# Performance work log

Measured on AMD Instinct MI355X. Metric: run time of the kernel, lower is better.

## Reference

```python
import jax, jax.numpy as jnp
import numpy as np

D_MODEL = 1024
NUM_HEADS = 16
D_K = D_MODEL // NUM_HEADS
LOCAL_WINDOW = 256
SCALE = 1.0 / np.float32(np.sqrt(D_K))
NEG = -1e9


def setup_inputs() -> dict:
    key = jax.random.key(0)
    ks = jax.random.split(key, 11)
    B, S, D = 2, 2048, D_MODEL
    s = 1.0 / np.float32(np.sqrt(D))
    return {
        "query": jax.random.normal(ks[0], (B, S, D), jnp.float32),
        "key": jax.random.normal(ks[1], (B, S, D), jnp.float32),
        "value": jax.random.normal(ks[2], (B, S, D), jnp.float32),
        "Wq": jax.random.normal(ks[3], (D, D), jnp.float32) * s,
        "bq": jnp.zeros((D,), jnp.float32),
        "Wk": jax.random.normal(ks[4], (D, D), jnp.float32) * s,
        "bk": jnp.zeros((D,), jnp.float32),
        "Wv": jax.random.normal(ks[5], (D, D), jnp.float32) * s,
        "bv": jnp.zeros((D,), jnp.float32),
        "Wo": jax.random.normal(ks[6], (D, D), jnp.float32) * s,
        "bo": jnp.zeros((D,), jnp.float32),
    }


def _band_mask(S):
    # torch loop: allowed cols j with max(0, i - w//2) <= j < min(S, i + w//2)
    i = jnp.arange(S)
    diff = i[None, :] - i[:, None]  # j - i
    half = LOCAL_WINDOW // 2
    return (diff >= -half) & (diff < half)  # [S, S] bool


def reference(query, key, value, Wq, bq, Wk, bk, Wv, bv, Wo, bo):
    B, S, D = query.shape
    H, dk = NUM_HEADS, D_K

    def proj(x, W, b):
        # nn.Linear: x @ W.T + b ; then split heads -> [B, H, S, dk]
        return (x @ W.T + b).reshape(B, S, H, dk).transpose(0, 2, 1, 3)

    Q = proj(query, Wq, bq)
    K = proj(key, Wk, bk)
    V = proj(value, Wv, bv)

    scores = jnp.einsum("bhqd,bhkd->bhqk", Q, K) * SCALE  # [B,H,S,S]
    band = _band_mask(S)
    scores = jnp.where(band[None, None, :, :], scores, NEG)
    attn = jax.nn.softmax(scores, axis=-1)
    out = jnp.einsum("bhqk,bhkd->bhqd", attn, V)  # [B,H,S,dk]
    out = out.transpose(0, 2, 1, 3).reshape(B, S, D)
    return out @ Wo.T + bo
```

## Files before the change

kernel.cpp:

```cpp
#include <hip/hip_runtime.h>
#include <stdint.h>

#define S_LEN 2048
#define NB 2
#define NH 16
#define DK 64
#define DM 1024
#define QK_SCALE 0.125f
#define NEG_BIG -1e30f

typedef __attribute__((ext_vector_type(8))) short bf16x8;
typedef __attribute__((ext_vector_type(4))) float f32x4;

static __device__ __forceinline__ f32x4 mfma16(bf16x8 a, bf16x8 b, f32x4 c) {
    return __builtin_amdgcn_mfma_f32_16x16x32_bf16(a, b, c, 0, 0, 0);
}

static __device__ __forceinline__ void gload_lds16(const void* g, void* l) {
    __builtin_amdgcn_global_load_lds((const __attribute__((address_space(1))) void*)g,
                                     (__attribute__((address_space(3))) void*)l,
                                     16, 0, 0);
}

static __device__ __forceinline__ unsigned short f2bf(float x) {
    unsigned int u = __float_as_uint(x);
    u += 0x7fffu + ((u >> 16) & 1u);
    return (unsigned short)(u >> 16);
}

struct CvtArgs {
    const float* src[7];
    unsigned short* dst[7];
    int n8[7];
};

__global__ __launch_bounds__(256) void cvt_f32_bf16(CvtArgs a) {
    const int t = blockIdx.y;
    const float* __restrict__ src = a.src[t];
    unsigned short* __restrict__ dst = a.dst[t];
    const int n8 = a.n8[t];
    const int stride = gridDim.x * blockDim.x;
    for (int i = blockIdx.x * blockDim.x + threadIdx.x; i < n8; i += stride) {
        float4 v0 = ((const float4*)src)[(size_t)i * 2];
        float4 v1 = ((const float4*)src)[(size_t)i * 2 + 1];
        union { bf16x8 v; unsigned short h[8]; } u;
        u.h[0] = f2bf(v0.x); u.h[1] = f2bf(v0.y); u.h[2] = f2bf(v0.z); u.h[3] = f2bf(v0.w);
        u.h[4] = f2bf(v1.x); u.h[5] = f2bf(v1.y); u.h[6] = f2bf(v1.z); u.h[7] = f2bf(v1.w);
        ((bf16x8*)dst)[i] = u.v;
    }
}

static __device__ __forceinline__ void gemm_core_128(
    const unsigned short* __restrict__ A,
    const unsigned short* __restrict__ W,
    unsigned short* sA, unsigned short* sB,
    int K, int m0, int n0, f32x4 acc[4][4])
{
    const int tid = threadIdx.x;
    const int wid = tid >> 6, lane = tid & 63;
    const int wr = wid >> 1, wc = wid & 1;
    const int fr = lane & 15, fg = lane >> 4;
    const int ldr = lane >> 3;
    const int ldc = ((lane & 7) ^ (lane >> 3)) * 8;

    const unsigned short* pA = A + (size_t)(m0 + ldr) * K + ldc;
    const unsigned short* pW = W + (size_t)(n0 + ldr) * K + ldc;

    const int cka0 = ((0 + fg) ^ (fr & 7)) * 8;
    const int cka1 = ((4 + fg) ^ (fr & 7)) * 8;

    for (int k0 = 0; k0 < K; k0 += 64) {
        __syncthreads();
        #pragma unroll
        for (int it = 0; it < 4; ++it) {
            const int rb = wid * 32 + it * 8;
            gload_lds16(pA + (size_t)(rb)*K + k0, sA + rb * 64);
            gload_lds16(pW + (size_t)(rb)*K + k0, sB + rb * 64);
        }
        __syncthreads();
        #pragma unroll
        for (int kf = 0; kf < 2; ++kf) {
            const int cka = kf ? cka1 : cka0;
            bf16x8 af[4], bfr[4];
            #pragma unroll
            for (int mf = 0; mf < 4; ++mf)
                af[mf] = *(const bf16x8*)(sA + (wr * 64 + mf * 16 + fr) * 64 + cka);
            #pragma unroll
            for (int nf = 0; nf < 4; ++nf)
                bfr[nf] = *(const bf16x8*)(sB + (wc * 64 + nf * 16 + fr) * 64 + cka);
            #pragma unroll
            for (int mf = 0; mf < 4; ++mf)
                #pragma unroll
                for (int nf = 0; nf < 4; ++nf)
                    acc[mf][nf] = mfma16(af[mf], bfr[nf], acc[mf][nf]);
        }
    }
}

__global__ __launch_bounds__(256, 3) void gemm_qkv(
    const unsigned short* __restrict__ Xq, const unsigned short* __restrict__ Xk,
    const unsigned short* __restrict__ Xv,
    const unsigned short* __restrict__ Wq, const unsigned short* __restrict__ Wk,
    const unsigned short* __restrict__ Wv,
    const float* __restrict__ bq, const float* __restrict__ bk, const float* __restrict__ bv,
    unsigned short* __restrict__ Qo, unsigned short* __restrict__ Ko,
    unsigned short* __restrict__ Vt)
{
    __shared__ unsigned short sA[128 * 64];
    __shared__ unsigned short sB[128 * 64];
    const int z = blockIdx.z;
    const unsigned short* A = (z == 0) ? Xq : ((z == 1) ? Xk : Xv);
    const unsigned short* W = (z == 0) ? Wq : ((z == 1) ? Wk : Wv);
    const float* bias = (z == 0) ? bq : ((z == 1) ? bk : bv);
    const int m0 = blockIdx.y * 128, n0 = blockIdx.x * 128;

    f32x4 acc[4][4] = {};
    gemm_core_128(A, W, sA, sB, DM, m0, n0, acc);

    const int tid = threadIdx.x, wid = tid >> 6, lane = tid & 63;
    const int wr = wid >> 1, wc = wid & 1, fr = lane & 15, fg = lane >> 4;
    unsigned short* Oh = (z == 0) ? Qo : Ko;
    #pragma unroll
    for (int nf = 0; nf < 4; ++nf) {
        const int col = n0 + wc * 64 + nf * 16 + fr;
        const float bb = bias[col];
        const int h = col >> 6, dd = col & (DK - 1);
        #pragma unroll
        for (int mf = 0; mf < 4; ++mf) {
            #pragma unroll
            for (int r = 0; r < 4; ++r) {
                const int row = m0 + wr * 64 + mf * 16 + fg * 4 + r;
                const int b = row >> 11, s = row & (S_LEN - 1);
                const float val = acc[mf][nf][r] + bb;
                if (z < 2)
                    Oh[(((size_t)b * NH + h) * S_LEN + s) * DK + dd] = f2bf(val);
                else
                    Vt[(((size_t)b * NH + h) * DK + dd) * S_LEN + s] = f2bf(val);
            }
        }
    }
}

__global__ __launch_bounds__(256, 2) void gemm_out(
    const unsigned short* __restrict__ A, const unsigned short* __restrict__ W,
    const float* __restrict__ bias, float* __restrict__ out)
{
    __shared__ unsigned short sA[64 * 64];
    __shared__ unsigned short sB[128 * 64];

    const int tid = threadIdx.x;
    const int wid = tid >> 6, lane = tid & 63;
    const int wr = wid >> 1, wc = wid & 1;
    const int fr = lane & 15, fg = lane >> 4;
    const int ldr = lane >> 3;
    const int ldc = ((lane & 7) ^ (lane >> 3)) * 8;
    const int m0 = blockIdx.y * 64, n0 = blockIdx.x * 128;

    const unsigned short* pA = A + (size_t)(m0 + ldr) * DM + ldc;
    const unsigned short* pW = W + (size_t)(n0 + ldr) * DM + ldc;

    const int cka0 = ((0 + fg) ^ (fr & 7)) * 8;
    const int cka1 = ((4 + fg) ^ (fr & 7)) * 8;

    f32x4 acc[2][4] = {};

    for (int k0 = 0; k0 < DM; k0 += 64) {
        __syncthreads();
        #pragma unroll
        for (int it = 0; it < 2; ++it) {
            const int rb = wid * 16 + it * 8;
            gload_lds16(pA + (size_t)rb * DM + k0, sA + rb * 64);
        }
        #pragma unroll
        for (int it = 0; it < 4; ++it) {
            const int rb = wid * 32 + it * 8;
            gload_lds16(pW + (size_t)rb * DM + k0, sB + rb * 64);
        }
        __syncthreads();
        #pragma unroll
        for (int kf = 0; kf < 2; ++kf) {
            const int cka = kf ? cka1 : cka0;
            bf16x8 af[2], bfr[4];
            #pragma unroll
            for (int mf = 0; mf < 2; ++mf)
                af[mf] = *(const bf16x8*)(sA + (wr * 32 + mf * 16 + fr) * 64 + cka);
            #pragma unroll
            for (int nf = 0; nf < 4; ++nf)
                bfr[nf] = *(const bf16x8*)(sB + (wc * 64 + nf * 16 + fr) * 64 + cka);
            #pragma unroll
            for (int mf = 0; mf < 2; ++mf)
                #pragma unroll
                for (int nf = 0; nf < 4; ++nf)
                    acc[mf][nf] = mfma16(af[mf], bfr[nf], acc[mf][nf]);
        }
    }

    #pragma unroll
    for (int nf = 0; nf < 4; ++nf) {
        const int col = n0 + wc * 64 + nf * 16 + fr;
        const float bb = bias[col];
        #pragma unroll
        for (int mf = 0; mf < 2; ++mf) {
            #pragma unroll
            for (int r = 0; r < 4; ++r) {
                const int row = m0 + wr * 32 + mf * 16 + fg * 4 + r;
                out[(size_t)row * DM + col] = acc[mf][nf][r] + bb;
            }
        }
    }
}

__global__ __launch_bounds__(256, 2) void attn_kernel(
    const unsigned short* __restrict__ Qb,
    const unsigned short* __restrict__ Kb,
    const unsigned short* __restrict__ Vt,
    unsigned short* __restrict__ Oout)
{
    __shared__ unsigned short sK[128 * 64];
    __shared__ unsigned short sV[64 * 128];
    __shared__ unsigned short sP[4][32 * 128];

    const int tid = threadIdx.x, wid = tid >> 6, lane = tid & 63;
    const int fr = lane & 15, fg = lane >> 4;
    const int qt = blockIdx.x, bh = blockIdx.y;
    const int q0 = qt * 128;
    const size_t base = (size_t)bh * (S_LEN * DK);

    bf16x8 qf[2][2];
    #pragma unroll
    for (int mf = 0; mf < 2; ++mf)
        #pragma unroll
        for (int kf = 0; kf < 2; ++kf)
            qf[mf][kf] = *(const bf16x8*)(Qb + base +
                (size_t)(q0 + wid * 32 + mf * 16 + fr) * DK + kf * 32 + fg * 8);

    f32x4 oacc[2][4] = {};
    float m_run[2][4], l_run[2][4];
    #pragma unroll
    for (int mf = 0; mf < 2; ++mf)
        #pragma unroll
        for (int r = 0; r < 4; ++r) { m_run[mf][r] = NEG_BIG; l_run[mf][r] = 0.f; }

    const int t_lo = (qt == 0) ? 1 : 0;
    const int t_hi = (qt == (S_LEN / 128 - 1)) ? 1 : 2;

    for (int t = t_lo; t <= t_hi; ++t) {
        const int kt0 = q0 + (t - 1) * 128;
        __syncthreads();
        {
            const unsigned short* gK = Kb + base + (size_t)kt0 * DK;
            #pragma unroll
            for (int it = 0; it < 4; ++it) {
                const int chunk = wid * 4 + it;
                gload_lds16(gK + chunk * 512 + lane * 8, sK + chunk * 512);
            }
            const unsigned short* gV = Vt + base + kt0;
            #pragma unroll
            for (int it = 0; it < 4; ++it) {
                const int chunk = wid * 4 + it;
                gload_lds16(gV + (size_t)(chunk * 4 + fg) * S_LEN + fr * 8, sV + chunk * 512);
            }
        }
        __syncthreads();

        f32x4 sacc[2][8] = {};
        #pragma unroll
        for (int kf = 0; kf < 2; ++kf) {
            bf16x8 kfr[8];
            #pragma unroll
            for (int nf = 0; nf < 8; ++nf)
                kfr[nf] = *(const bf16x8*)(sK + (nf * 16 + fr) * 64 + kf * 32 + fg * 8);
            #pragma unroll
            for (int mf = 0; mf < 2; ++mf)
                #pragma unroll
                for (int nf = 0; nf < 8; ++nf)
                    sacc[mf][nf] = mfma16(qf[mf][kf], kfr[nf], sacc[mf][nf]);
        }

        const int dt = (t - 1) * 128;
        #pragma unroll
        for (int mf = 0; mf < 2; ++mf) {
            #pragma unroll
            for (int r = 0; r < 4; ++r) {
                const int row = wid * 32 + mf * 16 + fg * 4 + r;
                float mm = NEG_BIG;
                #pragma unroll
                for (int nf = 0; nf < 8; ++nf) {
                    const int col = nf * 16 + fr;
                    const int diff = dt + col - row;
                    float s = sacc[mf][nf][r] * QK_SCALE;
                    s = (diff >= -128 && diff < 128) ? s : NEG_BIG;
                    sacc[mf][nf][r] = s;
                    mm = fmaxf(mm, s);
                }
                #pragma unroll
                for (int d = 1; d < 16; d <<= 1) mm = fmaxf(mm, __shfl_xor(mm, d));
                const float mold = m_run[mf][r];
                const float mn = fmaxf(mold, mm);
                m_run[mf][r] = mn;
                const float alpha = __expf(mold - mn);
                float ps = 0.f;
                #pragma unroll
                for (int nf = 0; nf < 8; ++nf) {
                    const float p = __expf(sacc[mf][nf][r] - mn);
                    ps += p;
                    sP[wid][(mf * 16 + fg * 4 + r) * 128 + nf * 16 + fr] = f2bf(p);
                }
                #pragma unroll
                for (int d = 1; d < 16; d <<= 1) ps += __shfl_xor(ps, d);
                l_run[mf][r] = l_run[mf][r] * alpha + ps;
                #pragma unroll
                for (int nf = 0; nf < 4; ++nf)
                    oacc[mf][nf][r] = oacc[mf][nf][r] * alpha;
            }
        }

        #pragma unroll
        for (int kf = 0; kf < 4; ++kf) {
            bf16x8 pa[2], vb[4];
            #pragma unroll
            for (int mf = 0; mf < 2; ++mf)
                pa[mf] = *(const bf16x8*)(&sP[wid][(mf * 16 + fr) * 128 + kf * 32 + fg * 8]);
            #pragma unroll
            for (int nf = 0; nf < 4; ++nf)
                vb[nf] = *(const bf16x8*)(sV + (nf * 16 + fr) * 128 + kf * 32 + fg * 8);
            #pragma unroll
            for (int mf = 0; mf < 2; ++mf)
                #pragma unroll
                for (int nf = 0; nf < 4; ++nf)
                    oacc[mf][nf] = mfma16(pa[mf], vb[nf], oacc[mf][nf]);
        }
    }

    const int b = bh >> 4, h = bh & 15;
    #pragma unroll
    for (int mf = 0; mf < 2; ++mf) {
        #pragma unroll
        for (int r = 0; r < 4; ++r) {
            const float inv = 1.0f / l_run[mf][r];
            const int token = b * S_LEN + q0 + wid * 32 + mf * 16 + fg * 4 + r;
            #pragma unroll
            for (int nf = 0; nf < 4; ++nf) {
                const int feat = h * 64 + nf * 16 + fr;
                Oout[(size_t)token * DM + feat] = f2bf(oacc[mf][nf][r] * inv);
            }
        }
    }
}

extern "C" void kernel_launch(void* const* d_in, const int* in_sizes, int n_in,
                              void* d_out, int out_size, void* d_ws, size_t ws_size,
                              hipStream_t stream)
{
    (void)in_sizes; (void)n_in; (void)out_size; (void)ws_size;
    const float* q  = (const float*)d_in[0];
    const float* k  = (const float*)d_in[1];
    const float* v  = (const float*)d_in[2];
    const float* Wq = (const float*)d_in[3];
    const float* bq = (const float*)d_in[4];
    const float* Wk = (const float*)d_in[5];
    const float* bk = (const float*)d_in[6];
    const float* Wv = (const float*)d_in[7];
    const float* bv = (const float*)d_in[8];
    const float* Wo = (const float*)d_in[9];
    const float* bo = (const float*)d_in[10];

    char* ws = (char*)d_ws;
    const size_t MB = 1024 * 1024;
    unsigned short* Xq  = (unsigned short*)(ws + 0 * MB);
    unsigned short* Xk  = (unsigned short*)(ws + 8 * MB);
    unsigned short* Xv  = (unsigned short*)(ws + 16 * MB);
    unsigned short* Qb  = (unsigned short*)(ws + 24 * MB);
    unsigned short* Kb  = (unsigned short*)(ws + 32 * MB);
    unsigned short* Vt  = (unsigned short*)(ws + 40 * MB);
    unsigned short* Wqb = (unsigned short*)(ws + 48 * MB);
    unsigned short* Wkb = (unsigned short*)(ws + 50 * MB);
    unsigned short* Wvb = (unsigned short*)(ws + 52 * MB);
    unsigned short* Wob = (unsigned short*)(ws + 54 * MB);
    unsigned short* AO  = Xq;

    CvtArgs ca;
    ca.src[0] = q;  ca.dst[0] = Xq;  ca.n8[0] = (NB * S_LEN * DM) / 8;
    ca.src[1] = k;  ca.dst[1] = Xk;  ca.n8[1] = (NB * S_LEN * DM) / 8;
    ca.src[2] = v;  ca.dst[2] = Xv;  ca.n8[2] = (NB * S_LEN * DM) / 8;
    ca.src[3] = Wq; ca.dst[3] = Wqb; ca.n8[3] = (DM * DM) / 8;
    ca.src[4] = Wk; ca.dst[4] = Wkb; ca.n8[4] = (DM * DM) / 8;
    ca.src[5] = Wv; ca.dst[5] = Wvb; ca.n8[5] = (DM * DM) / 8;
    ca.src[6] = Wo; ca.dst[6] = Wob; ca.n8[6] = (DM * DM) / 8;
    cvt_f32_bf16<<<dim3(1024, 7), 256, 0, stream>>>(ca);

    gemm_qkv<<<dim3(DM / 128, (NB * S_LEN) / 128, 3), 256, 0, stream>>>(
        Xq, Xk, Xv, Wqb, Wkb, Wvb, bq, bk, bv, Qb, Kb, Vt);

    attn_kernel<<<dim3(S_LEN / 128, NB * NH), 256, 0, stream>>>(Qb, Kb, Vt, AO);

    gemm_out<<<dim3(DM / 128, (NB * S_LEN) / 64), 256, 0, stream>>>(
        AO, Wob, bo, (float*)d_out);
}
```

Before: 109.1 us.

## Double-buffer LDS tiles in QKV projection GEMM to overlap loads with MFMA

Rewrites the QKV GEMM main loop to use two LDS buffers, prefetching the next K-tile via direct global-to-LDS loads while computing on the current one, with explicit vmcnt waits and barriers. This hides global load latency behind MFMA work instead of fully serializing load and compute. LDS doubles to 64KB per block, so launch bounds drop occupancy from 3 to 2 blocks per CU.

```diff
diff --git a/kernel.cpp b/kernel.cpp
--- a/kernel.cpp
+++ b/kernel.cpp
@@ -50,54 +50,7 @@
     }
 }
 
-static __device__ __forceinline__ void gemm_core_128(
-    const unsigned short* __restrict__ A,
-    const unsigned short* __restrict__ W,
-    unsigned short* sA, unsigned short* sB,
-    int K, int m0, int n0, f32x4 acc[4][4])
-{
-    const int tid = threadIdx.x;
-    const int wid = tid >> 6, lane = tid & 63;
-    const int wr = wid >> 1, wc = wid & 1;
-    const int fr = lane & 15, fg = lane >> 4;
-    const int ldr = lane >> 3;
-    const int ldc = ((lane & 7) ^ (lane >> 3)) * 8;
-
-    const unsigned short* pA = A + (size_t)(m0 + ldr) * K + ldc;
-    const unsigned short* pW = W + (size_t)(n0 + ldr) * K + ldc;
-
-    const int cka0 = ((0 + fg) ^ (fr & 7)) * 8;
-    const int cka1 = ((4 + fg) ^ (fr & 7)) * 8;
-
-    for (int k0 = 0; k0 < K; k0 += 64) {
-        __syncthreads();
-        #pragma unroll
-        for (int it = 0; it < 4; ++it) {
-            const int rb = wid * 32 + it * 8;
-            gload_lds16(pA + (size_t)(rb)*K + k0, sA + rb * 64);
-            gload_lds16(pW + (size_t)(rb)*K + k0, sB + rb * 64);
-        }
-        __syncthreads();
-        #pragma unroll
-        for (int kf = 0; kf < 2; ++kf) {
-            const int cka = kf ? cka1 : cka0;
-            bf16x8 af[4], bfr[4];
-            #pragma unroll
-            for (int mf = 0; mf < 4; ++mf)
-                af[mf] = *(const bf16x8*)(sA + (wr * 64 + mf * 16 + fr) * 64 + cka);
-            #pragma unroll
-            for (int nf = 0; nf < 4; ++nf)
-                bfr[nf] = *(const bf16x8*)(sB + (wc * 64 + nf * 16 + fr) * 64 + cka);
-            #pragma unroll
-            for (int mf = 0; mf < 4; ++mf)
-                #pragma unroll
-                for (int nf = 0; nf < 4; ++nf)
-                    acc[mf][nf] = mfma16(af[mf], bfr[nf], acc[mf][nf]);
-        }
-    }
-}
-
-__global__ __launch_bounds__(256, 3) void gemm_qkv(
+__global__ __launch_bounds__(256, 2) void gemm_qkv(
     const unsigned short* __restrict__ Xq, const unsigned short* __restrict__ Xk,
     const unsigned short* __restrict__ Xv,
     const unsigned short* __restrict__ Wq, const unsigned short* __restrict__ Wk,
@@ -106,19 +59,76 @@
     unsigned short* __restrict__ Qo, unsigned short* __restrict__ Ko,
     unsigned short* __restrict__ Vt)
 {
-    __shared__ unsigned short sA[128 * 64];
-    __shared__ unsigned short sB[128 * 64];
+    __shared__ unsigned short lds[32768];
+
+    const int tid = threadIdx.x;
+    const int wid = tid >> 6, lane = tid & 63;
+    const int wr = wid >> 1, wc = wid & 1;
+    const int fr = lane & 15, fg = lane >> 4;
     const int z = blockIdx.z;
+    const int m0 = blockIdx.y * 128, n0 = blockIdx.x * 128;
+
     const unsigned short* A = (z == 0) ? Xq : ((z == 1) ? Xk : Xv);
     const unsigned short* W = (z == 0) ? Wq : ((z == 1) ? Wk : Wv);
     const float* bias = (z == 0) ? bq : ((z == 1) ? bk : bv);
-    const int m0 = blockIdx.y * 128, n0 = blockIdx.x * 128;
+
+    const int ldr = lane >> 3;
+    const int ldc = ((lane & 7) ^ (lane >> 3)) * 8;
+    const unsigned short* pA = A + (size_t)(m0 + ldr) * DM + ldc;
+    const unsigned short* pW = W + (size_t)(n0 + ldr) * DM + ldc;
+
+    const int cka0 = ((0 + fg) ^ (fr & 7)) * 8;
+    const int cka1 = ((4 + fg) ^ (fr & 7)) * 8;
 
     f32x4 acc[4][4] = {};
-    gemm_core_128(A, W, sA, sB, DM, m0, n0, acc);
-
-    const int tid = threadIdx.x, wid = tid >> 6, lane = tid & 63;
-    const int wr = wid >> 1, wc = wid & 1, fr = lane & 15, fg = lane >> 4;
+
+    #define STAGE_QKV(T, B)                                                     \
+        do {                                                                    \
+            const int _k0 = (T) * 64;                                           \
+            unsigned short* _dA = lds + (B) * 16384;                            \
+            unsigned short* _dB = lds + (B) * 16384 + 8192;                     \
+            _Pragma("unroll")                                                   \
+            for (int _it = 0; _it < 4; ++_it) {                                 \
+                const int _rb = wid * 32 + _it * 8;                             \
+                gload_lds16(pA + (size_t)_rb * DM + _k0, _dA + _rb * 64);       \
+                gload_lds16(pW + (size_t)_rb * DM + _k0, _dB + _rb * 64);       \
+            }                                                                   \
+        } while (0)
+
+    STAGE_QKV(0, 0);
+
+    for (int t = 0; t < 16; ++t) {
+        const int b = t & 1;
+        if (t < 15) {
+            STAGE_QKV(t + 1, b ^ 1);
+            asm volatile("s_waitcnt vmcnt(8)" ::: "memory");
+        } else {
+            asm volatile("s_waitcnt vmcnt(0)" ::: "memory");
+        }
+        asm volatile("s_barrier" ::: "memory");
+
+        const unsigned short* sA = lds + b * 16384;
+        const unsigned short* sB = sA + 8192;
+        #pragma unroll
+        for (int kf = 0; kf < 2; ++kf) {
+            const int cka = kf ? cka1 : cka0;
+            bf16x8 af[4], bfr[4];
+            #pragma unroll
+            for (int mf = 0; mf < 4; ++mf)
+                af[mf] = *(const bf16x8*)(sA + (wr * 64 + mf * 16 + fr) * 64 + cka);
+            #pragma unroll
+            for (int nf = 0; nf < 4; ++nf)
+                bfr[nf] = *(const bf16x8*)(sB + (wc * 64 + nf * 16 + fr) * 64 + cka);
+            #pragma unroll
+            for (int mf = 0; mf < 4; ++mf)
+                #pragma unroll
+                for (int nf = 0; nf < 4; ++nf)
+                    acc[mf][nf] = mfma16(af[mf], bfr[nf], acc[mf][nf]);
+        }
+        asm volatile("s_barrier" ::: "memory");
+    }
+    #undef STAGE_QKV
+
     unsigned short* Oh = (z == 0) ? Qo : Ko;
     #pragma unroll
     for (int nf = 0; nf < 4; ++nf) {
@@ -130,12 +140,12 @@
             #pragma unroll
             for (int r = 0; r < 4; ++r) {
                 const int row = m0 + wr * 64 + mf * 16 + fg * 4 + r;
-                const int b = row >> 11, s = row & (S_LEN - 1);
+                const int bb_ = row >> 11, s = row & (S_LEN - 1);
                 const float val = acc[mf][nf][r] + bb;
                 if (z < 2)
-                    Oh[(((size_t)b * NH + h) * S_LEN + s) * DK + dd] = f2bf(val);
+                    Oh[(((size_t)bb_ * NH + h) * S_LEN + s) * DK + dd] = f2bf(val);
                 else
-                    Vt[(((size_t)b * NH + h) * DK + dd) * S_LEN + s] = f2bf(val);
+                    Vt[(((size_t)bb_ * NH + h) * DK + dd) * S_LEN + s] = f2bf(val);
             }
         }
     }
```

Result: no change. 108.4 us (-0.7%).
